# Kernel tuning notes

Hardware: AMD Instinct MI355X
Metric: run time of the kernel (lower is better)

## Reference

```python
import jax, jax.numpy as jnp
import numpy as np

EPS = 1e-12  # F.normalize default eps


def _l2_normalize(x):
    n = jnp.linalg.norm(x, axis=-1, keepdims=True)
    return x / jnp.maximum(n, EPS)


def setup_inputs() -> dict:
    key = jax.random.key(0)
    k1, k2 = jax.random.split(key)
    B, N, D = 2048, 100000, 256
    query = jax.random.normal(k1, (B, D), dtype=jnp.float32)
    memory_states = jax.random.normal(k2, (N, D), dtype=jnp.float32)
    return {"query": query, "memory_states": memory_states, "k": 8}


def reference(query, memory_states, k):
    # cosine-similarity retrieval: normalize both sides, dense matmul, top-k, gather
    mem_norm = _l2_normalize(memory_states)          # [N, D]
    query_norm = _l2_normalize(query)                # [B, D]
    scores = query_norm @ mem_norm.T                 # [B, N]
    top_k_scores, indices = jax.lax.top_k(scores, k)  # [B, k] each
    retrieved = memory_states[indices]               # [B, k, D] (raw, un-normalized states as in torch)
    return retrieved, top_k_scores
```

## Files before the change

### kernel.cpp

```cpp
#include <hip/hip_runtime.h>
#include <hip/hip_bf16.h>
#include <stdint.h>

#define DIM 256
#define TOPK 8
#define NSTRIPS 64
#define STRIP_TOP 8
#define QT 256
#define NT 32
#define CAND (NSTRIPS * STRIP_TOP)
#define RESCORE 64
#define IDXMASK 0x1FFFFu

typedef __attribute__((ext_vector_type(8))) short short8;
typedef __attribute__((ext_vector_type(4))) float floatx4;
typedef __attribute__((address_space(3))) unsigned int lds_u32;
typedef __attribute__((address_space(1))) const unsigned int gbl_u32;

__device__ __forceinline__ unsigned short f2bf(float f) {
    union { float f; uint32_t u; } v; v.f = f;
    uint32_t u = v.u;
    uint32_t r = u + 0x7fffu + ((u >> 16) & 1u);
    return (unsigned short)(r >> 16);
}

__device__ __forceinline__ uint32_t umaxu(uint32_t a, uint32_t b) { return a > b ? a : b; }
__device__ __forceinline__ uint32_t uminu(uint32_t a, uint32_t b) { return a < b ? a : b; }

__device__ __forceinline__ void top8_insert(uint32_t* ts, uint32_t key) {
#pragma unroll
    for (int j = 0; j < STRIP_TOP - 1; j++) {
        uint32_t m;
        asm("v_med3_u32 %0, %1, %2, %3" : "=v"(m) : "v"(ts[j]), "v"(ts[j + 1]), "v"(key));
        ts[j] = m;
    }
    ts[STRIP_TOP - 1] = umaxu(ts[STRIP_TOP - 1], key);
}

__global__ void prep_kernel(const float* __restrict__ query,
                            const float* __restrict__ mem,
                            float* __restrict__ rnorm_mem,
                            unsigned short* __restrict__ q_bf16,
                            unsigned short* __restrict__ mem_bf16,
                            int B, int N)
{
    int wave = threadIdx.x >> 6;
    int lane = threadIdx.x & 63;
    int row  = blockIdx.x * 4 + wave;
    int total = N + B;
    if (row >= total) return;
    const float* src = (row < N) ? (mem + (size_t)row * DIM)
                                 : (query + (size_t)(row - N) * DIM);
    float4 v = ((const float4*)src)[lane];
    float ss = v.x * v.x + v.y * v.y + v.z * v.z + v.w * v.w;
#pragma unroll
    for (int m = 32; m >= 1; m >>= 1) ss += __shfl_xor(ss, m, 64);
    float rinv = 1.0f / fmaxf(sqrtf(ss), 1e-12f);
    ushort4 o;
    o.x = f2bf(v.x * rinv); o.y = f2bf(v.y * rinv);
    o.z = f2bf(v.z * rinv); o.w = f2bf(v.w * rinv);
    if (row < N) {
        if (lane == 0) rnorm_mem[row] = rinv;
        if (mem_bf16) ((ushort4*)(mem_bf16 + (size_t)row * DIM))[lane] = o;
    } else {
        ((ushort4*)(q_bf16 + (size_t)(row - N) * DIM))[lane] = o;
    }
}

template<bool PRE>
__global__ __launch_bounds__(512, 4) void score_select_kernel(
    const float* __restrict__ mem,
    const float* __restrict__ rnorm_mem,
    const unsigned short* __restrict__ mem_bf16,
    const unsigned short* __restrict__ q_bf16,
    uint32_t* __restrict__ cand_key,
    int B, int N)
{
    __shared__ unsigned short lds_m[4][NT * DIM];

    const int t    = threadIdx.x;
    const int wave = t >> 6;
    const int lane = t & 63;
    const int quad = lane >> 4;
    const int l16  = lane & 15;

    const int lin  = (int)(blockIdx.x + gridDim.x * blockIdx.y);
    const int SPX  = NSTRIPS / 8;
    const int strip = (lin & 7) * SPX + ((lin >> 3) % SPX);
    const int qb    = (lin >> 3) / SPX;
    const int qbase = qb * QT;

    const int SS    = (N + NSTRIPS - 1) / NSTRIPS;
    const int n0    = strip * SS;
    const int nend  = (n0 + SS < N) ? (n0 + SS) : N;
    const int limit = nend - n0;
    const int ntiles = (limit + NT - 1) / NT;

    short8 qfrag[2][8];
#pragma unroll
    for (int b = 0; b < 2; b++) {
        int qrow = qbase + wave * 32 + b * 16 + l16;
        const unsigned short* qp = q_bf16 + (size_t)qrow * DIM + quad * 8;
#pragma unroll
        for (int ks = 0; ks < 8; ks++)
            qfrag[b][ks] = *(const short8*)(qp + ks * 32);
    }

    uint32_t ts[2][STRIP_TOP];
#pragma unroll
    for (int b = 0; b < 2; b++)
#pragma unroll
        for (int j = 0; j < STRIP_TOP; j++) ts[b][j] = 0;

    const int l5  = lane >> 5;
    const int s32 = lane & 31;

    const int o0 = l16 * 512 + (quad ^ (l16 & 3)) * 16 + ((l16 >> 2) & 1) * 64;
    const int o1 = o0 ^ 64;

    auto stage = [&](unsigned short* lbase, int tileIdx) {
        int base = n0 + tileIdx * NT;
        if (PRE) {
#pragma unroll
            for (int is = 0; is < 2; is++) {
                int rl = is * 16 + wave * 2 + l5;
                int n = base + rl; if (n >= nend) n = nend - 1;
                int chunk = s32 ^ (rl & 7);
                const unsigned short* gp = mem_bf16 + (size_t)n * DIM + chunk * 8;
                unsigned short* lp = lbase + (is * 16 + wave * 2) * DIM;
                __builtin_amdgcn_global_load_lds((gbl_u32*)(const void*)gp,
                                                 (lds_u32*)(void*)lp, 16, 0, 0);
            }
        } else {
#pragma unroll
            for (int i = 0; i < 4; i++) {
                int rl = i * 8 + wave;
                int n = base + rl;
                ushort4 o;
                if (n < nend) {
                    float rinv = rnorm_mem[n];
                    float4 v = ((const float4*)(mem + (size_t)n * DIM))[lane];
                    o.x = f2bf(v.x * rinv); o.y = f2bf(v.y * rinv);
                    o.z = f2bf(v.z * rinv); o.w = f2bf(v.w * rinv);
                } else { o.x = 0; o.y = 0; o.z = 0; o.w = 0; }
                int slot = (lane >> 1) ^ (rl & 7);
                *(ushort4*)(lbase + rl * DIM + slot * 8 + (lane & 1) * 4) = o;
            }
        }
    };

    const floatx4 bias4 = {1.125f, 1.125f, 1.125f, 1.125f};

    auto compute_tile = [&](const unsigned short* lbuf, int tile) {
        floatx4 acc[2][2];
#pragma unroll
        for (int a = 0; a < 2; a++)
#pragma unroll
            for (int b = 0; b < 2; b++) acc[a][b] = bias4;

        const char* pb0 = (const char*)lbuf + o0;
        const char* pb1 = (const char*)lbuf + o1;
#pragma unroll
        for (int ks = 0; ks < 8; ks++) {
#pragma unroll
            for (int a = 0; a < 2; a++) {
                const char* p = (ks & 1) ? pb1 : pb0;
                short8 m = *(const short8*)(p + a * 8192 + (ks >> 1) * 128);
#pragma unroll
                for (int b = 0; b < 2; b++)
                    acc[a][b] = __builtin_amdgcn_mfma_f32_16x16x32_bf16(m, qfrag[b][ks], acc[a][b], 0, 0, 0);
            }
        }

        const int tb0 = tile * NT + quad * 4;
        const bool full = (tile * NT + NT <= limit);
#pragma unroll
        for (int b = 0; b < 2; b++) {
#pragma unroll
            for (int a = 0; a < 2; a++) {
#pragma unroll
                for (int rp = 0; rp < 2; rp++) {
                    int loc0 = tb0 + a * 16 + 2 * rp;
                    uint32_t k0 = (__float_as_uint(acc[a][b][2 * rp])     & 0xFFFF0000u) | (uint32_t)loc0;
                    uint32_t k1 = (__float_as_uint(acc[a][b][2 * rp + 1]) & 0xFFFF0000u) | (uint32_t)(loc0 + 1);
                    if (!full) {
                        if (loc0 >= limit)     k0 = 0;
                        if (loc0 + 1 >= limit) k1 = 0;
                    }
                    uint32_t kmax = umaxu(k0, k1);
                    uint32_t kmin = uminu(k0, k1);
                    top8_insert(ts[b], kmax);
                    if (__any(kmin > ts[b][0]))
                        top8_insert(ts[b], kmin);
                }
            }
        }
    };

    stage(&lds_m[0][0], 0);
    if (1 < ntiles) stage(&lds_m[1][0], 1);
    __syncthreads();

    for (int tp = 0; tp < ntiles; tp += 2) {
        if (tp + 2 < ntiles) stage(&lds_m[(tp + 2) & 3][0], tp + 2);
        if (tp + 3 < ntiles) stage(&lds_m[(tp + 3) & 3][0], tp + 3);
        compute_tile(&lds_m[tp & 3][0], tp);
        if (tp + 1 < ntiles) compute_tile(&lds_m[(tp + 1) & 3][0], tp + 1);
        __syncthreads();
    }

#pragma unroll
    for (int b = 0; b < 2; b++) {
#pragma unroll
        for (int step = 32; step >= 16; step >>= 1) {
            uint32_t other[STRIP_TOP];
#pragma unroll
            for (int j = 0; j < STRIP_TOP; j++)
                other[j] = __shfl_xor(ts[b][j], step, 64);
#pragma unroll
            for (int j = 0; j < STRIP_TOP; j++)
                top8_insert(ts[b], other[j]);
        }
    }

    if (quad == 0) {
#pragma unroll
        for (int b = 0; b < 2; b++) {
            int q = qbase + wave * 32 + b * 16 + l16;
            size_t off = ((size_t)q * NSTRIPS + strip) * STRIP_TOP;
            uint4 o0v, o1v;
            uint32_t k;
            k = ts[b][0]; o0v.x = ((k >> 17) << 17) | (uint32_t)(n0 + (int)(k & 0xFFFFu));
            k = ts[b][1]; o0v.y = ((k >> 17) << 17) | (uint32_t)(n0 + (int)(k & 0xFFFFu));
            k = ts[b][2]; o0v.z = ((k >> 17) << 17) | (uint32_t)(n0 + (int)(k & 0xFFFFu));
            k = ts[b][3]; o0v.w = ((k >> 17) << 17) | (uint32_t)(n0 + (int)(k & 0xFFFFu));
            k = ts[b][4]; o1v.x = ((k >> 17) << 17) | (uint32_t)(n0 + (int)(k & 0xFFFFu));
            k = ts[b][5]; o1v.y = ((k >> 17) << 17) | (uint32_t)(n0 + (int)(k & 0xFFFFu));
            k = ts[b][6]; o1v.z = ((k >> 17) << 17) | (uint32_t)(n0 + (int)(k & 0xFFFFu));
            k = ts[b][7]; o1v.w = ((k >> 17) << 17) | (uint32_t)(n0 + (int)(k & 0xFFFFu));
            ((uint4*)(cand_key + off))[0] = o0v;
            ((uint4*)(cand_key + off))[1] = o1v;
        }
    }
}

__global__ __launch_bounds__(256) void rescore_kernel(
    const float* __restrict__ query,
    const float* __restrict__ mem,
    const uint32_t* __restrict__ cand_key,
    float* __restrict__ out,
    int B, int N)
{
    __shared__ uint32_t cs[CAND];
    __shared__ float  lds_q[DIM];
    __shared__ double red[4];
    __shared__ double qss_sh;
    __shared__ int    sel_i[RESCORE];
    __shared__ double rs[RESCORE];
    __shared__ double best_s[TOPK];
    __shared__ int    best_i[TOPK];

    const int t    = threadIdx.x;
    const int q    = blockIdx.x;
    const int lane = t & 63;
    const int wave = t >> 6;

    for (int i = t; i < CAND; i += 256)
        cs[i] = cand_key[(size_t)q * CAND + i];

    float qv = query[(size_t)q * DIM + t];
    lds_q[t] = qv;
    double p = (double)qv * (double)qv;
#pragma unroll
    for (int m = 32; m >= 1; m >>= 1) p += __shfl_xor(p, m, 64);
    if (lane == 0) red[wave] = p;
    __syncthreads();
    if (t == 0) qss_sh = red[0] + red[1] + red[2] + red[3];

    {
        uint32_t* qcs = cs + wave * 128;
        for (int k = 2; k <= 128; k <<= 1) {
            for (int j = k >> 1; j > 0; j >>= 1) {
                int i  = 2 * lane - (lane & (j - 1));
                int ip = i + j;
                bool up = ((i & k) == 0);
                uint32_t a = qcs[i], b2 = qcs[ip];
                bool aFirst = a > b2;
                bool doSwap = up ? (!aFirst) : aFirst;
                if (doSwap) { qcs[i] = b2; qcs[ip] = a; }
            }
        }
        if (lane < 16) sel_i[wave * 16 + lane] = (int)(qcs[lane] & IDXMASK);
    }
    __syncthreads();

    double qss = qss_sh;
    for (int r = 0; r < 16; r++) {
        int c = wave * 16 + r;
        int idx = sel_i[c];
        float4 mv = ((const float4*)(mem + (size_t)idx * DIM))[lane];
        float4 qv4 = ((const float4*)lds_q)[lane];
        double dqm = (double)mv.x * (double)qv4.x + (double)mv.y * (double)qv4.y
                   + (double)mv.z * (double)qv4.z + (double)mv.w * (double)qv4.w;
        double dmm = (double)mv.x * (double)mv.x + (double)mv.y * (double)mv.y
                   + (double)mv.z * (double)mv.z + (double)mv.w * (double)mv.w;
#pragma unroll
        for (int m = 32; m >= 1; m >>= 1) {
            dqm += __shfl_xor(dqm, m, 64);
            dmm += __shfl_xor(dmm, m, 64);
        }
        if (lane == 0)
            rs[c] = dqm / (fmax(sqrt(qss), 1e-12) * fmax(sqrt(dmm), 1e-12));
    }
    __syncthreads();

    if (t == 0) {
        double bs[TOPK]; int bi[TOPK];
        for (int i = 0; i < TOPK; i++) { bs[i] = -1e300; bi[i] = 0x7fffffff; }
        for (int c = 0; c < RESCORE; c++) {
            double s = rs[c]; int id = sel_i[c];
            bool better = (s > bs[TOPK - 1]) || (s == bs[TOPK - 1] && id < bi[TOPK - 1]);
            if (better) {
                int pos = TOPK - 1;
                while (pos > 0) {
                    bool b2 = (s > bs[pos - 1]) || (s == bs[pos - 1] && id < bi[pos - 1]);
                    if (!b2) break;
                    bs[pos] = bs[pos - 1]; bi[pos] = bi[pos - 1]; pos--;
                }
                bs[pos] = s; bi[pos] = id;
            }
        }
        for (int i = 0; i < TOPK; i++) { best_s[i] = bs[i]; best_i[i] = bi[i]; }
    }
    __syncthreads();

    size_t score_base = (size_t)B * TOPK * DIM;
    if (t < TOPK) out[score_base + (size_t)q * TOPK + t] = (float)best_s[t];

#pragma unroll
    for (int rep = 0; rep < 2; rep++) {
        int j  = t >> 5;
        int d4 = (t & 31) + rep * 32;
        int idx = best_i[j];
        float4 v = ((const float4*)(mem + (size_t)idx * DIM))[d4];
        ((float4*)(out + ((size_t)q * TOPK + j) * DIM))[d4] = v;
    }
}

extern "C" void kernel_launch(void* const* d_in, const int* in_sizes, int n_in,
                              void* d_out, int out_size, void* d_ws, size_t ws_size,
                              hipStream_t stream)
{
    const float* query = (const float*)d_in[0];
    const float* mem   = (const float*)d_in[1];
    int B = in_sizes[0] / DIM;
    int N = in_sizes[1] / DIM;

    auto align256 = [](size_t x) { return (x + 255) & ~(size_t)255; };
    size_t off = 0;
    auto alloc = [&](size_t bytes) { void* p = (char*)d_ws + off; off += align256(bytes); return p; };

    float* rnorm_mem       = (float*)alloc((size_t)N * 4);
    unsigned short* q_bf16 = (unsigned short*)alloc((size_t)B * DIM * 2);
    uint32_t* cand_key     = (uint32_t*)alloc((size_t)B * CAND * 4);
    size_t base_need = off;
    unsigned short* mem_bf16 = (unsigned short*)((char*)d_ws + base_need);
    bool pre = (base_need + align256((size_t)N * DIM * 2)) <= ws_size;
    if (!pre) mem_bf16 = nullptr;

    int prep_blocks = (N + B + 3) / 4;
    prep_kernel<<<prep_blocks, 256, 0, stream>>>(query, mem, rnorm_mem, q_bf16,
                                                 mem_bf16, B, N);

    dim3 g2((B + QT - 1) / QT, NSTRIPS);
    if (pre)
        score_select_kernel<true><<<g2, 512, 0, stream>>>(mem, rnorm_mem, mem_bf16, q_bf16,
                                                          cand_key, B, N);
    else
        score_select_kernel<false><<<g2, 512, 0, stream>>>(mem, rnorm_mem, mem_bf16, q_bf16,
                                                           cand_key, B, N);

    rescore_kernel<<<B, 256, 0, stream>>>(query, mem, cand_key, (float*)d_out, B, N);
}
```

Before: 345.6 us.

## Halve tile height and use a 5-slot LDS ring with partial vmcnt waits

```diff
diff --git a/kernel.cpp b/kernel.cpp
--- a/kernel.cpp
+++ b/kernel.cpp
@@ -7,7 +7,8 @@
 #define NSTRIPS 64
 #define STRIP_TOP 8
 #define QT 256
-#define NT 32
+#define NT 16
+#define RING 5
 #define CAND (NSTRIPS * STRIP_TOP)
 #define RESCORE 64
 #define IDXMASK 0x1FFFFu
@@ -76,7 +77,7 @@
     uint32_t* __restrict__ cand_key,
     int B, int N)
 {
-    __shared__ unsigned short lds_m[4][NT * DIM];
+    __shared__ unsigned short lds_m[RING][NT * DIM];
 
     const int t    = threadIdx.x;
     const int wave = t >> 6;
@@ -121,19 +122,16 @@
     auto stage = [&](unsigned short* lbase, int tileIdx) {
         int base = n0 + tileIdx * NT;
         if (PRE) {
-#pragma unroll
-            for (int is = 0; is < 2; is++) {
-                int rl = is * 16 + wave * 2 + l5;
-                int n = base + rl; if (n >= nend) n = nend - 1;
-                int chunk = s32 ^ (rl & 7);
-                const unsigned short* gp = mem_bf16 + (size_t)n * DIM + chunk * 8;
-                unsigned short* lp = lbase + (is * 16 + wave * 2) * DIM;
-                __builtin_amdgcn_global_load_lds((gbl_u32*)(const void*)gp,
-                                                 (lds_u32*)(void*)lp, 16, 0, 0);
-            }
+            int rl = wave * 2 + l5;
+            int n = base + rl; if (n >= nend) n = nend - 1;
+            int chunk = s32 ^ (rl & 7);
+            const unsigned short* gp = mem_bf16 + (size_t)n * DIM + chunk * 8;
+            unsigned short* lp = lbase + wave * 2 * DIM;
+            __builtin_amdgcn_global_load_lds((gbl_u32*)(const void*)gp,
+                                             (lds_u32*)(void*)lp, 16, 0, 0);
         } else {
 #pragma unroll
-            for (int i = 0; i < 4; i++) {
+            for (int i = 0; i < 2; i++) {
                 int rl = i * 8 + wave;
                 int n = base + rl;
                 ushort4 o;
@@ -152,24 +150,19 @@
     const floatx4 bias4 = {1.125f, 1.125f, 1.125f, 1.125f};
 
     auto compute_tile = [&](const unsigned short* lbuf, int tile) {
-        floatx4 acc[2][2];
-#pragma unroll
-        for (int a = 0; a < 2; a++)
-#pragma unroll
-            for (int b = 0; b < 2; b++) acc[a][b] = bias4;
+        floatx4 acc[2];
+#pragma unroll
+        for (int b = 0; b < 2; b++) acc[b] = bias4;
 
         const char* pb0 = (const char*)lbuf + o0;
         const char* pb1 = (const char*)lbuf + o1;
 #pragma unroll
         for (int ks = 0; ks < 8; ks++) {
-#pragma unroll
-            for (int a = 0; a < 2; a++) {
-                const char* p = (ks & 1) ? pb1 : pb0;
-                short8 m = *(const short8*)(p + a * 8192 + (ks >> 1) * 128);
-#pragma unroll
-                for (int b = 0; b < 2; b++)
-                    acc[a][b] = __builtin_amdgcn_mfma_f32_16x16x32_bf16(m, qfrag[b][ks], acc[a][b], 0, 0, 0);
-            }
+            const char* p = (ks & 1) ? pb1 : pb0;
+            short8 m = *(const short8*)(p + (ks >> 1) * 128);
+#pragma unroll
+            for (int b = 0; b < 2; b++)
+                acc[b] = __builtin_amdgcn_mfma_f32_16x16x32_bf16(m, qfrag[b][ks], acc[b], 0, 0, 0);
         }
 
         const int tb0 = tile * NT + quad * 4;
@@ -177,36 +170,48 @@
 #pragma unroll
         for (int b = 0; b < 2; b++) {
 #pragma unroll
-            for (int a = 0; a < 2; a++) {
-#pragma unroll
-                for (int rp = 0; rp < 2; rp++) {
-                    int loc0 = tb0 + a * 16 + 2 * rp;
-                    uint32_t k0 = (__float_as_uint(acc[a][b][2 * rp])     & 0xFFFF0000u) | (uint32_t)loc0;
-                    uint32_t k1 = (__float_as_uint(acc[a][b][2 * rp + 1]) & 0xFFFF0000u) | (uint32_t)(loc0 + 1);
-                    if (!full) {
-                        if (loc0 >= limit)     k0 = 0;
-                        if (loc0 + 1 >= limit) k1 = 0;
-                    }
-                    uint32_t kmax = umaxu(k0, k1);
-                    uint32_t kmin = uminu(k0, k1);
-                    top8_insert(ts[b], kmax);
-                    if (__any(kmin > ts[b][0]))
-                        top8_insert(ts[b], kmin);
+            for (int rp = 0; rp < 2; rp++) {
+                int loc0 = tb0 + 2 * rp;
+                uint32_t k0 = (__float_as_uint(acc[b][2 * rp])     & 0xFFFF0000u) | (uint32_t)loc0;
+                uint32_t k1 = (__float_as_uint(acc[b][2 * rp + 1]) & 0xFFFF0000u) | (uint32_t)(loc0 + 1);
+                if (!full) {
+                    if (loc0 >= limit)     k0 = 0;
+                    if (loc0 + 1 >= limit) k1 = 0;
                 }
+                uint32_t kmax = umaxu(k0, k1);
+                uint32_t kmin = uminu(k0, k1);
+                top8_insert(ts[b], kmax);
+                if (__any(kmin > ts[b][0]))
+                    top8_insert(ts[b], kmin);
             }
         }
     };
 
-    stage(&lds_m[0][0], 0);
-    if (1 < ntiles) stage(&lds_m[1][0], 1);
-    __syncthreads();
-
-    for (int tp = 0; tp < ntiles; tp += 2) {
-        if (tp + 2 < ntiles) stage(&lds_m[(tp + 2) & 3][0], tp + 2);
-        if (tp + 3 < ntiles) stage(&lds_m[(tp + 3) & 3][0], tp + 3);
-        compute_tile(&lds_m[tp & 3][0], tp);
-        if (tp + 1 < ntiles) compute_tile(&lds_m[(tp + 1) & 3][0], tp + 1);
-        __syncthreads();
+    for (int i = 0; i < 3 && i < ntiles; i++) stage(&lds_m[i][0], i);
+
+    int cur = 0, nxt = 3 % RING;
+    for (int tl = 0; tl < ntiles; tl++) {
+        if (tl + 3 < ntiles) {
+            stage(&lds_m[nxt][0], tl + 3);
+            if (PRE) {
+                asm volatile("s_waitcnt vmcnt(3)" ::: "memory");
+                __builtin_amdgcn_s_barrier();
+                __builtin_amdgcn_sched_barrier(0);
+            } else {
+                __syncthreads();
+            }
+        } else {
+            if (PRE) {
+                asm volatile("s_waitcnt vmcnt(0)" ::: "memory");
+                __builtin_amdgcn_s_barrier();
+                __builtin_amdgcn_sched_barrier(0);
+            } else {
+                __syncthreads();
+            }
+        }
+        compute_tile(&lds_m[cur][0], tl);
+        cur = (cur + 1 == RING) ? 0 : cur + 1;
+        nxt = (nxt + 1 == RING) ? 0 : nxt + 1;
     }
 
 #pragma unroll
```

Result: slower. 354.2 us (+2.5%).
